# Kernel tuning notes

Measured on AMD Instinct MI355X. Metric: run time of the kernel, lower is better.

The kernel has to match this reference:

```python
import jax, jax.numpy as jnp
import numpy as np

D_MODEL = 2048
NUM_HEADS = 16
HEAD_DIM = D_MODEL // NUM_HEADS  # 128; scale uses head_dim even though attention is over full d_model
B, S = 2, 2048


def setup_inputs() -> dict:
    key = jax.random.key(0)
    ks = jax.random.split(key, 5)
    x = jax.random.normal(ks[0], (B, S, D_MODEL), dtype=jnp.float32)
    # causal additive mask, as typically passed to this module (2D, sliced mask[-s:, :kv])
    neg = jnp.float32(-1e9)
    mask = jnp.where(jnp.triu(jnp.ones((S, S), dtype=bool), k=1), neg, jnp.float32(0.0))
    std = 1.0 / np.sqrt(D_MODEL)
    Wq = jax.random.normal(ks[1], (D_MODEL, D_MODEL), dtype=jnp.float32) * std
    Wk = jax.random.normal(ks[2], (D_MODEL, D_MODEL), dtype=jnp.float32) * std
    Wv = jax.random.normal(ks[3], (D_MODEL, D_MODEL), dtype=jnp.float32) * std
    Wo = jax.random.normal(ks[4], (D_MODEL, D_MODEL), dtype=jnp.float32) * std
    return {"x": x, "mask": mask, "Wq": Wq, "Wk": Wk, "Wv": Wv, "Wo": Wo}


def reference(x, mask, Wq, Wk, Wv, Wo):
    # nn.Linear(bias=False): y = x @ W^T
    q = jnp.einsum('bsd,ed->bse', x, Wq)  # [B,S,D]
    k = jnp.einsum('bsd,ed->bse', x, Wk)
    v = jnp.einsum('bsd,ed->bse', x, Wv)
    scale = jnp.float32(HEAD_DIM ** -0.5)
    # NOTE: faithful to source — contraction over full d_model, no head split
    scores = jnp.einsum('bsd,btd->bst', q, k) * scale  # [B,S,S]
    scores = scores + mask  # mask[-s:, :kv] == mask here (s == kv)
    weights = jax.nn.softmax(scores, axis=-1)
    out = jnp.einsum('bst,btd->bsd', weights, v)
    return jnp.einsum('bsd,ed->bse', out, Wo)
```

## Files before the change

### kernel.cpp

```cpp
#include <hip/hip_runtime.h>

#define DM  2048
#define SQ  2048
#define NB  2
#define BSZ (NB * SQ)

typedef _Float16 f16x8 __attribute__((ext_vector_type(8)));
typedef __attribute__((ext_vector_type(4))) float f32x4;

#define ASG(p) (const __attribute__((address_space(1))) void*)(p)
#define ASL(p) (__attribute__((address_space(3))) void*)(p)

__device__ __forceinline__ unsigned short f2h(float f) {
  union { _Float16 h; unsigned short u; } x;
  x.h = (_Float16)f;
  return x.u;
}
__device__ __forceinline__ float h2f(unsigned short u) {
  union { unsigned short u; _Float16 h; } x;
  x.u = u;
  return (float)x.h;
}

__global__ __launch_bounds__(256) void cast_all(const float4* __restrict__ x,
                                                const float4* __restrict__ wq,
                                                const float4* __restrict__ wk,
                                                const float4* __restrict__ wv,
                                                const float4* __restrict__ wo,
                                                ushort4* __restrict__ out,
                                                int n4x, int n4w) {
  int i = blockIdx.x * 256 + threadIdx.x;
  float4 v;
  if (i < n4x) {
    v = x[i];
  } else {
    int j = i - n4x;
    int seg = j >> 20;
    int off = j & (n4w - 1);
    const float4* src = (seg == 0) ? wq : (seg == 1) ? wk : (seg == 2) ? wv : wo;
    v = src[off];
  }
  ushort4 h;
  h.x = f2h(v.x); h.y = f2h(v.y); h.z = f2h(v.z); h.w = f2h(v.w);
  out[i] = h;
}

#define SB() __builtin_amdgcn_sched_barrier(0)
#define BARX() do { SB(); __builtin_amdgcn_s_barrier(); SB(); } while (0)

#define STAGEK(BUFL, REG, U, T) do { \
    const unsigned short* G_ = (REG) ? Bb : Ab; \
    const int ldG_ = (REG) ? ldB : ldA; \
    const int r0_ = ((REG) ? bn0 : bm0) + (U) * 32; \
    const long k0_ = (long)((T) << 6); \
    char* db_ = ldsb + (BUFL) * 32768 + (REG) * 16384 + (U) * 4096 + tid * 16; \
    const unsigned short* s_ = G_ + (long)(r0_ + srow) * ldG_ + k0_ + scsw; \
    __builtin_amdgcn_global_load_lds(ASG(s_), ASL(db_), 16, 0, 0); \
  } while (0)

#define LDAK(BUFL, MH, Af) do { \
    const char* ba_ = ldsb + (BUFL) * 32768 + (wm * 64 + (MH) * 32) * 128 + arow; \
    _Pragma("unroll") for (int mm_ = 0; mm_ < 2; mm_++) { \
      Af[mm_][0] = *(const f16x8*)(ba_ + mm_ * 2048 + sl0); \
      Af[mm_][1] = *(const f16x8*)(ba_ + mm_ * 2048 + sl1); } \
  } while (0)

#define LDBK(BUFL, NH, Bf) do { \
    const char* bb_ = ldsb + (BUFL) * 32768 + 16384 + (wn * 64 + (NH) * 32) * 128 + arow; \
    _Pragma("unroll") for (int nn_ = 0; nn_ < 2; nn_++) { \
      Bf[nn_][0] = *(const f16x8*)(bb_ + nn_ * 2048 + sl0); \
      Bf[nn_][1] = *(const f16x8*)(bb_ + nn_ * 2048 + sl1); } \
  } while (0)

#define PHK(Af, Bf, MH, NH) do { \
    __builtin_amdgcn_s_setprio(1); \
    _Pragma("unroll") for (int mm_ = 0; mm_ < 2; mm_++) \
    _Pragma("unroll") for (int nn_ = 0; nn_ < 2; nn_++) \
    _Pragma("unroll") for (int ks_ = 0; ks_ < 2; ks_++) \
      acc[(MH) * 2 + mm_][(NH) * 2 + nn_] = __builtin_amdgcn_mfma_f32_16x16x32_f16( \
          Af[mm_][ks_], Bf[nn_][ks_], acc[(MH) * 2 + mm_][(NH) * 2 + nn_], 0, 0, 0); \
    __builtin_amdgcn_s_setprio(0); \
  } while (0)

#define GROUPK(BUFL, T) do { \
    LDAK(BUFL, 0, a0); LDBK(BUFL, 0, b0); \
    LDAK(BUFL, 1, a1); \
    if ((T) + 1 < NT) { STAGEK((BUFL) ^ 1, 1, 2, (T) + 1); STAGEK((BUFL) ^ 1, 1, 3, (T) + 1); } \
    PHK(a0, b0, 0, 0); \
    BARX(); \
    LDBK(BUFL, 1, b1); \
    PHK(a1, b0, 1, 0); \
    BARX(); \
    if ((T) + 2 < NT) { STAGEK(BUFL, 0, 0, (T) + 2); STAGEK(BUFL, 0, 1, (T) + 2); \
                        STAGEK(BUFL, 0, 2, (T) + 2); STAGEK(BUFL, 0, 3, (T) + 2); } \
    PHK(a1, b1, 1, 1); \
    BARX(); \
    if ((T) + 2 < NT) { STAGEK(BUFL, 1, 0, (T) + 2); STAGEK(BUFL, 1, 1, (T) + 2); } \
    PHK(a0, b1, 0, 1); \
    SB(); \
    if ((T) + 1 < NT) { \
      if ((T) + 1 == NT - 1) { asm volatile("s_waitcnt vmcnt(0)" ::: "memory"); } \
      else                   { asm volatile("s_waitcnt vmcnt(6)" ::: "memory"); } \
    } \
    __builtin_amdgcn_s_barrier(); \
    SB(); \
  } while (0)

template <int OM>
__device__ __forceinline__ void gemm128_body(
    char* ldsb, const unsigned short* __restrict__ Ab,
    const unsigned short* __restrict__ Bb,
    float* __restrict__ Cf, unsigned short* __restrict__ Ch, long cb,
    int NT, int ldA, int ldB, int ldC, int bm0, int bn0, float alpha) {
  const int tid = threadIdx.x, lane = tid & 63, wid = tid >> 6;
  const int wm = wid >> 1, wn = wid & 1;
  const int fr = lane & 15, fq = lane >> 4;

  const int sl0 = ((fq ^ (fr & 7)) << 4);
  const int sl1 = (((4 + fq) ^ (fr & 7)) << 4);
  const int arow = fr << 7;

  const int srow = tid >> 3;
  const int scsw = ((tid & 7) ^ (srow & 7)) << 3;

  f32x4 acc[4][4];
#pragma unroll
  for (int m = 0; m < 4; m++)
#pragma unroll
    for (int n = 0; n < 4; n++)
#pragma unroll
      for (int r = 0; r < 4; r++) acc[m][n][r] = 0.f;

  f16x8 a0[2][2], a1[2][2], b0[2][2], b1[2][2];

  STAGEK(0, 0, 0, 0); STAGEK(0, 0, 1, 0); STAGEK(0, 0, 2, 0); STAGEK(0, 0, 3, 0);
  STAGEK(0, 1, 0, 0); STAGEK(0, 1, 1, 0); STAGEK(0, 1, 2, 0); STAGEK(0, 1, 3, 0);
  STAGEK(1, 0, 0, 1); STAGEK(1, 0, 1, 1); STAGEK(1, 0, 2, 1); STAGEK(1, 0, 3, 1);
  STAGEK(1, 1, 0, 1); STAGEK(1, 1, 1, 1);
  asm volatile("s_waitcnt vmcnt(6)" ::: "memory");
  __builtin_amdgcn_s_barrier();
  SB();

  for (int t = 0; t < NT; t += 2) {
    GROUPK(0, t);
    GROUPK(1, t + 1);
  }

#pragma unroll
  for (int mh = 0; mh < 2; mh++)
#pragma unroll
    for (int mm = 0; mm < 2; mm++)
#pragma unroll
      for (int nh = 0; nh < 2; nh++)
#pragma unroll
        for (int nn = 0; nn < 2; nn++) {
          const int col = bn0 + wn * 64 + nh * 32 + nn * 16 + fr;
#pragma unroll
          for (int r = 0; r < 4; r++) {
            const long row = (long)bm0 + wm * 64 + mh * 32 + mm * 16 + fq * 4 + r;
            const long ci = cb + row * ldC + col;
            const float vv = acc[mh * 2 + mm][nh * 2 + nn][r] * alpha;
            if constexpr (OM == 0) Cf[ci] = vv;
            else                   Ch[ci] = f2h(vv);
          }
        }
}

template <int OM, int CAUSAL>
__global__ __launch_bounds__(256, 2) void gemm128(
    const unsigned short* __restrict__ A, const unsigned short* __restrict__ B,
    float* __restrict__ Cf, unsigned short* __restrict__ Ch,
    int K, long sAb, long sBb, long sCb,
    int ldA, int ldB, int ldC, float alpha) {
  __shared__ __align__(16) char ldsarr[65536];
  const int bm0 = blockIdx.x * 128;
  const int bn0 = blockIdx.y * 128;
  const int z = blockIdx.z;
  int NT = K >> 6;
  if (CAUSAL == 2) NT = (bm0 + 128) >> 6;
  gemm128_body<OM>(ldsarr, A + (long)z * sAb, B + (long)z * sBb,
                   Cf, Ch, (long)z * sCb, NT, ldA, ldB, ldC, bm0, bn0, alpha);
}

__global__ __launch_bounds__(256, 2) void k_scores_vtt(
    const unsigned short* __restrict__ qk, unsigned short* __restrict__ scores,
    const unsigned short* __restrict__ wv, const unsigned short* __restrict__ x16,
    unsigned short* __restrict__ vTT, float scale) {
  __shared__ __align__(16) char ldsarr[65536];
  const int bm0 = blockIdx.x * 128;
  const int bn0 = blockIdx.y * 128;
  if (blockIdx.z < 2) {
    if (blockIdx.y >= SQ / 128) return;
    if (bn0 > bm0) return;
    const long z = blockIdx.z;
    gemm128_body<1>(ldsarr, qk + z * (long)SQ * 2 * DM, qk + DM + z * (long)SQ * 2 * DM,
                    nullptr, scores, z * (long)SQ * SQ,
                    DM >> 6, 2 * DM, 2 * DM, SQ, bm0, bn0, scale);
  } else {
    gemm128_body<1>(ldsarr, wv, x16, nullptr, vTT, 0L,
                    DM >> 6, DM, DM, BSZ, bm0, bn0, 1.0f);
  }
}

__global__ __launch_bounds__(256) void softmax_causal(const unsigned short* __restrict__ sc,
                                                      unsigned short* __restrict__ pr) {
  const int row = blockIdx.x;
  const int s = row & (SQ - 1);
  const long base = (long)row * SQ;
  const int n = s + 1;
  const int tid = threadIdx.x;
  const int lane = tid & 63;
  const int wv = tid >> 6;
  const int e0 = tid * 8;
  __shared__ float red[4];

  union { uint4 u4; unsigned short us[8]; } in, ou;
  in.u4 = *(const uint4*)&sc[base + e0];

  float v[8];
  float mx = -3.0e38f;
#pragma unroll
  for (int j = 0; j < 8; j++) {
    v[j] = (e0 + j < n) ? h2f(in.us[j]) : -3.0e38f;
    mx = fmaxf(mx, v[j]);
  }
#pragma unroll
  for (int o = 32; o >= 1; o >>= 1) mx = fmaxf(mx, __shfl_xor(mx, o));
  if (lane == 0) red[wv] = mx;
  __syncthreads();
  mx = fmaxf(fmaxf(red[0], red[1]), fmaxf(red[2], red[3]));
  __syncthreads();

  float sum = 0.f;
#pragma unroll
  for (int j = 0; j < 8; j++) {
    v[j] = (e0 + j < n) ? __expf(v[j] - mx) : 0.f;
    sum += v[j];
  }
#pragma unroll
  for (int o = 32; o >= 1; o >>= 1) sum += __shfl_xor(sum, o);
  if (lane == 0) red[wv] = sum;
  __syncthreads();
  const float inv = 1.f / (red[0] + red[1] + red[2] + red[3]);
#pragma unroll
  for (int j = 0; j < 8; j++) ou.us[j] = (e0 + j < n) ? f2h(v[j] * inv) : (unsigned short)0;
  *(uint4*)&pr[base + e0] = ou.u4;
}

extern "C" void kernel_launch(void* const* d_in, const int* in_sizes, int n_in,
                              void* d_out, int out_size, void* d_ws, size_t ws_size,
                              hipStream_t stream) {
  (void)in_sizes; (void)n_in; (void)out_size; (void)ws_size;
  const float* x  = (const float*)d_in[0];
  const float* Wq = (const float*)d_in[2];
  const float* Wk = (const float*)d_in[3];
  const float* Wv = (const float*)d_in[4];
  const float* Wo = (const float*)d_in[5];
  float* out = (float*)d_out;

  const long ELx = (long)BSZ * DM;
  const long ELw = (long)DM * DM;

  char* ws = (char*)d_ws;
  size_t off = 0;
  auto take = [&](size_t bytes) { void* p = ws + off; off += bytes; return p; };

  unsigned short* x16   = (unsigned short*)take(ELx * 2);
  unsigned short* wqk16 = (unsigned short*)take(2 * ELw * 2);
  unsigned short* wv16  = (unsigned short*)take(ELw * 2);
  unsigned short* wo16  = (unsigned short*)take(ELw * 2);
  unsigned short* qk16  = (unsigned short*)take((long)BSZ * 2 * DM * 2);
  unsigned short* vTT   = (unsigned short*)take(ELx * 2);
  unsigned short* probs = (unsigned short*)take((long)NB * SQ * SQ * 2);
  unsigned short* scores = wqk16;
  unsigned short* ctx = qk16;
  unsigned short* q16 = qk16;
  unsigned short* k16 = qk16 + DM;
  (void)q16; (void)k16;

  const int n4x = (int)(ELx / 4), n4w = (int)(ELw / 4);
  cast_all<<<dim3((n4x + 4 * n4w) / 256), 256, 0, stream>>>(
      (const float4*)x, (const float4*)Wq, (const float4*)Wk,
      (const float4*)Wv, (const float4*)Wo, (ushort4*)x16, n4x, n4w);

  const float scale = 0.08838834764831845f;

  gemm128<1, 0><<<dim3(BSZ / 128, 2 * DM / 128, 1), 256, 0, stream>>>(
      x16, wqk16, nullptr, qk16, DM, 0L, 0L, 0L, DM, DM, 2 * DM, 1.0f);

  k_scores_vtt<<<dim3(SQ / 128, BSZ / 128, 3), 256, 0, stream>>>(
      qk16, scores, wv16, x16, vTT, scale);

  softmax_causal<<<dim3(NB * SQ), 256, 0, stream>>>(scores, probs);

  gemm128<1, 2><<<dim3(SQ / 128, DM / 128, NB), 256, 0, stream>>>(
      probs, vTT, nullptr, ctx, SQ, (long)SQ * SQ, 2048L, (long)SQ * DM,
      SQ, BSZ, DM, 1.0f);
  gemm128<0, 0><<<dim3(BSZ / 128, DM / 128, 1), 256, 0, stream>>>(
      ctx, wo16, out, nullptr, DM, 0L, 0L, 0L, DM, DM, DM, 1.0f);
}
```

Baseline: 237.1 us.

## Precompute Wq^T·Wk and Wo·Wv products to drop projection and output GEMMs

Reassociates the attention computation: scores are formed as (x·Wq^T·Wk)·x^T using a precomputed weight product, and the value and output projections are merged into one weight product G=Wo·Wv so the PV GEMM writes the final fp32 output directly. This removes the separate Q/K projection of width 2*DM and the final Wo GEMM, cutting total GEMM FLOPs. It adds weight-weight GEMMs each call, a transposing fp16 cast kernel, and extra rounding from storing fused weight matrices in fp16.

```diff
diff --git a/kernel.cpp b/kernel.cpp
--- a/kernel.cpp
+++ b/kernel.cpp
@@ -22,27 +22,55 @@
   return (float)x.h;
 }
 
-__global__ __launch_bounds__(256) void cast_all(const float4* __restrict__ x,
-                                                const float4* __restrict__ wq,
-                                                const float4* __restrict__ wk,
-                                                const float4* __restrict__ wv,
-                                                const float4* __restrict__ wo,
-                                                ushort4* __restrict__ out,
-                                                int n4x, int n4w) {
+__global__ __launch_bounds__(256) void cast_x_wo(const float4* __restrict__ x,
+                                                 const float4* __restrict__ wo,
+                                                 ushort4* __restrict__ outx,
+                                                 ushort4* __restrict__ outwo,
+                                                 int n4x, int n4w) {
   int i = blockIdx.x * 256 + threadIdx.x;
   float4 v;
-  if (i < n4x) {
-    v = x[i];
-  } else {
-    int j = i - n4x;
-    int seg = j >> 20;
-    int off = j & (n4w - 1);
-    const float4* src = (seg == 0) ? wq : (seg == 1) ? wk : (seg == 2) ? wv : wo;
-    v = src[off];
-  }
+  ushort4* dst;
+  int j;
+  if (i < n4x) { v = x[i]; dst = outx; j = i; }
+  else { j = i - n4x; if (j >= n4w) return; v = wo[j]; dst = outwo; }
   ushort4 h;
   h.x = f2h(v.x); h.y = f2h(v.y); h.z = f2h(v.z); h.w = f2h(v.w);
-  out[i] = h;
+  dst[j] = h;
+}
+
+__global__ __launch_bounds__(256) void cast_t(const float* __restrict__ wq,
+                                              const float* __restrict__ wk,
+                                              const float* __restrict__ wv,
+                                              unsigned short* __restrict__ wqT,
+                                              unsigned short* __restrict__ wkT,
+                                              unsigned short* __restrict__ wvT) {
+  __shared__ unsigned short tile[64][66];
+  const float* in = (blockIdx.z == 0) ? wq : (blockIdx.z == 1) ? wk : wv;
+  unsigned short* outT = (blockIdx.z == 0) ? wqT : (blockIdx.z == 1) ? wkT : wvT;
+  const int tid = threadIdx.x;
+  const int d0 = blockIdx.x * 64, e0 = blockIdx.y * 64;
+  const int r = tid >> 4;
+  const int c = (tid & 15) * 4;
+#pragma unroll
+  for (int p = 0; p < 4; p++) {
+    const int dl = r + p * 16;
+    float4 v = *(const float4*)&in[(long)(d0 + dl) * DM + e0 + c];
+    tile[c + 0][dl] = f2h(v.x);
+    tile[c + 1][dl] = f2h(v.y);
+    tile[c + 2][dl] = f2h(v.z);
+    tile[c + 3][dl] = f2h(v.w);
+  }
+  __syncthreads();
+  const int r2 = tid >> 3;
+  const int c2 = (tid & 7) * 8;
+#pragma unroll
+  for (int p = 0; p < 2; p++) {
+    const int el = r2 + p * 32;
+    union { uint4 u4; unsigned short us[8]; } o;
+#pragma unroll
+    for (int k = 0; k < 8; k++) o.us[k] = tile[el][c2 + k];
+    *(uint4*)&outT[(long)(e0 + el) * DM + d0 + c2] = o.u4;
+  }
 }
 
 #define SB() __builtin_amdgcn_sched_barrier(0)
@@ -175,6 +203,7 @@
   __shared__ __align__(16) char ldsarr[65536];
   const int bm0 = blockIdx.x * 128;
   const int bn0 = blockIdx.y * 128;
+  if (CAUSAL == 1 && bn0 > bm0) return;
   const int z = blockIdx.z;
   int NT = K >> 6;
   if (CAUSAL == 2) NT = (bm0 + 128) >> 6;
@@ -182,23 +211,32 @@
                    Cf, Ch, (long)z * sCb, NT, ldA, ldB, ldC, bm0, bn0, alpha);
 }
 
-__global__ __launch_bounds__(256, 2) void k_scores_vtt(
-    const unsigned short* __restrict__ qk, unsigned short* __restrict__ scores,
-    const unsigned short* __restrict__ wv, const unsigned short* __restrict__ x16,
-    unsigned short* __restrict__ vTT, float scale) {
+__global__ __launch_bounds__(256, 2) void k_mt_g(
+    const unsigned short* __restrict__ wkT, const unsigned short* __restrict__ wqT,
+    const unsigned short* __restrict__ wo16, const unsigned short* __restrict__ wvT,
+    unsigned short* __restrict__ MT, unsigned short* __restrict__ G) {
   __shared__ __align__(16) char ldsarr[65536];
   const int bm0 = blockIdx.x * 128;
   const int bn0 = blockIdx.y * 128;
-  if (blockIdx.z < 2) {
-    if (blockIdx.y >= SQ / 128) return;
-    if (bn0 > bm0) return;
-    const long z = blockIdx.z;
-    gemm128_body<1>(ldsarr, qk + z * (long)SQ * 2 * DM, qk + DM + z * (long)SQ * 2 * DM,
-                    nullptr, scores, z * (long)SQ * SQ,
-                    DM >> 6, 2 * DM, 2 * DM, SQ, bm0, bn0, scale);
+  if (blockIdx.z == 0)
+    gemm128_body<1>(ldsarr, wkT, wqT, nullptr, MT, 0L, DM >> 6, DM, DM, DM, bm0, bn0, 1.0f);
+  else
+    gemm128_body<1>(ldsarr, wo16, wvT, nullptr, G, 0L, DM >> 6, DM, DM, DM, bm0, bn0, 1.0f);
+}
+
+__global__ __launch_bounds__(256, 2) void k_y_ut(
+    const unsigned short* __restrict__ x16, const unsigned short* __restrict__ MT,
+    const unsigned short* __restrict__ G,
+    unsigned short* __restrict__ y, unsigned short* __restrict__ uT) {
+  __shared__ __align__(16) char ldsarr[65536];
+  if (blockIdx.z == 0) {
+    const int bm0 = blockIdx.x * 128;
+    const int bn0 = blockIdx.y * 128;
+    gemm128_body<1>(ldsarr, x16, MT, nullptr, y, 0L, DM >> 6, DM, DM, DM, bm0, bn0, 1.0f);
   } else {
-    gemm128_body<1>(ldsarr, wv, x16, nullptr, vTT, 0L,
-                    DM >> 6, DM, DM, BSZ, bm0, bn0, 1.0f);
+    const int bm0 = blockIdx.y * 128;
+    const int bn0 = blockIdx.x * 128;
+    gemm128_body<1>(ldsarr, G, x16, nullptr, uT, 0L, DM >> 6, DM, DM, BSZ, bm0, bn0, 1.0f);
   }
 }
 
@@ -265,37 +303,37 @@
   size_t off = 0;
   auto take = [&](size_t bytes) { void* p = ws + off; off += bytes; return p; };
 
-  unsigned short* x16   = (unsigned short*)take(ELx * 2);
-  unsigned short* wqk16 = (unsigned short*)take(2 * ELw * 2);
-  unsigned short* wv16  = (unsigned short*)take(ELw * 2);
-  unsigned short* wo16  = (unsigned short*)take(ELw * 2);
-  unsigned short* qk16  = (unsigned short*)take((long)BSZ * 2 * DM * 2);
-  unsigned short* vTT   = (unsigned short*)take(ELx * 2);
+  unsigned short* x16  = (unsigned short*)take(ELx * 2);
+  unsigned short* wqT  = (unsigned short*)take(ELw * 2);
+  unsigned short* wkT  = (unsigned short*)take(ELw * 2);
+  unsigned short* wvT  = (unsigned short*)take(ELw * 2);
+  unsigned short* wo16 = (unsigned short*)take(ELw * 2);
+  unsigned short* MT   = (unsigned short*)take(ELw * 2);
+  unsigned short* G    = (unsigned short*)take(ELw * 2);
+  unsigned short* y    = (unsigned short*)take(ELx * 2);
+  unsigned short* uT   = (unsigned short*)take(ELx * 2);
   unsigned short* probs = (unsigned short*)take((long)NB * SQ * SQ * 2);
-  unsigned short* scores = wqk16;
-  unsigned short* ctx = qk16;
-  unsigned short* q16 = qk16;
-  unsigned short* k16 = qk16 + DM;
-  (void)q16; (void)k16;
+  unsigned short* scores = wqT;
 
   const int n4x = (int)(ELx / 4), n4w = (int)(ELw / 4);
-  cast_all<<<dim3((n4x + 4 * n4w) / 256), 256, 0, stream>>>(
-      (const float4*)x, (const float4*)Wq, (const float4*)Wk,
-      (const float4*)Wv, (const float4*)Wo, (ushort4*)x16, n4x, n4w);
+  cast_x_wo<<<dim3((n4x + n4w + 255) / 256), 256, 0, stream>>>(
+      (const float4*)x, (const float4*)Wo, (ushort4*)x16, (ushort4*)wo16, n4x, n4w);
+  cast_t<<<dim3(DM / 64, DM / 64, 3), 256, 0, stream>>>(
+      Wq, Wk, Wv, wqT, wkT, wvT);
 
   const float scale = 0.08838834764831845f;
 
-  gemm128<1, 0><<<dim3(BSZ / 128, 2 * DM / 128, 1), 256, 0, stream>>>(
-      x16, wqk16, nullptr, qk16, DM, 0L, 0L, 0L, DM, DM, 2 * DM, 1.0f);
-
-  k_scores_vtt<<<dim3(SQ / 128, BSZ / 128, 3), 256, 0, stream>>>(
-      qk16, scores, wv16, x16, vTT, scale);
+  k_mt_g<<<dim3(DM / 128, DM / 128, 2), 256, 0, stream>>>(
+      wkT, wqT, wo16, wvT, MT, G);
+  k_y_ut<<<dim3(BSZ / 128, DM / 128, 2), 256, 0, stream>>>(
+      x16, MT, G, y, uT);
+  gemm128<1, 1><<<dim3(SQ / 128, SQ / 128, NB), 256, 0, stream>>>(
+      y, x16, nullptr, scores, DM, (long)SQ * DM, (long)SQ * DM,
+      (long)SQ * SQ, DM, DM, SQ, scale);
 
   softmax_causal<<<dim3(NB * SQ), 256, 0, stream>>>(scores, probs);
 
-  gemm128<1, 2><<<dim3(SQ / 128, DM / 128, NB), 256, 0, stream>>>(
-      probs, vTT, nullptr, ctx, SQ, (long)SQ * SQ, 2048L, (long)SQ * DM,
+  gemm128<0, 2><<<dim3(SQ / 128, DM / 128, NB), 256, 0, stream>>>(
+      probs, uT, out, nullptr, SQ, (long)SQ * SQ, 2048L, (long)SQ * DM,
       SQ, BSZ, DM, 1.0f);
-  gemm128<0, 0><<<dim3(BSZ / 128, DM / 128, 1), 256, 0, stream>>>(
-      ctx, wo16, out, nullptr, DM, 0L, 0L, 0L, DM, DM, DM, 1.0f);
-}
+}
```

Result: faster. 208.4 us (-12.1%).
